# Performance work log

Hardware: AMD Instinct MI355X
Metric: run time of the kernel (lower is better)

## Reference

```python
import jax, jax.numpy as jnp
import numpy as np


def setup_inputs() -> dict:
    key = jax.random.key(0)
    k1, k2 = jax.random.split(key)
    N = 2_000_000
    rotation = jax.random.normal(k1, (N, 3, 3), dtype=jnp.float32)
    # learned parameter: eye(3) + 0.001 * randn(3,3)
    mat = jnp.eye(3, dtype=jnp.float32) + 0.001 * jax.random.normal(k2, (3, 3), dtype=jnp.float32)
    return {"rotation": rotation, "mat": mat}


def reference(rotation, mat):
    # new_mat[n] = rotation[n] @ mat   (mat broadcast over the batch)
    new_mat = jnp.einsum('nab,bc->nac', rotation, mat)
    # batched 3x3 SVD; polar orthogonal factor U @ V^T
    U, S, Vh = jnp.linalg.svd(new_mat, full_matrices=False)
    out = jnp.einsum('nab,nbc->nac', U, Vh)  # Vh is already V^T
    logdet = jnp.zeros((rotation.shape[0],), dtype=rotation.dtype)
    return out, logdet
```

## Files before the change

kernel.cpp:

```cpp
#include <hip/hip_runtime.h>
#include <math.h>

constexpr int BLOCK = 256;

__global__ __launch_bounds__(BLOCK) void polar3x3_kernel(
    const float* __restrict__ rot,
    const float* __restrict__ mat,
    float* __restrict__ outq,
    float* __restrict__ logdet,
    int N)
{
    const long long idx = (long long)blockIdx.x * BLOCK + threadIdx.x;
    if (idx >= N) return;

    const float* rp = rot + idx * 9;
    const float r0=rp[0], r1=rp[1], r2=rp[2], r3=rp[3], r4=rp[4],
                r5=rp[5], r6=rp[6], r7=rp[7], r8=rp[8];

    const float m0=mat[0], m1=mat[1], m2=mat[2], m3=mat[3], m4=mat[4],
                m5=mat[5], m6=mat[6], m7=mat[7], m8=mat[8];

    float x0 = fmaf(r0,m0, fmaf(r1,m3, r2*m6));
    float x1 = fmaf(r0,m1, fmaf(r1,m4, r2*m7));
    float x2 = fmaf(r0,m2, fmaf(r1,m5, r2*m8));
    float x3 = fmaf(r3,m0, fmaf(r4,m3, r5*m6));
    float x4 = fmaf(r3,m1, fmaf(r4,m4, r5*m7));
    float x5 = fmaf(r3,m2, fmaf(r4,m5, r5*m8));
    float x6 = fmaf(r6,m0, fmaf(r7,m3, r8*m6));
    float x7 = fmaf(r6,m1, fmaf(r7,m4, r8*m7));
    float x8 = fmaf(r6,m2, fmaf(r7,m5, r8*m8));

    const double dR = (double)r0*((double)r4*r8 - (double)r5*r7)
                    - (double)r1*((double)r3*r8 - (double)r5*r6)
                    + (double)r2*((double)r3*r7 - (double)r4*r6);
    const double dM = (double)m0*((double)m4*m8 - (double)m5*m7)
                    - (double)m1*((double)m3*m8 - (double)m5*m6)
                    + (double)m2*((double)m3*m7 - (double)m4*m6);
    const float detA = (float)(dR * dM);

    #pragma unroll
    for (int it = 0; it < 6; ++it) {
        const float c0 = fmaf(x4,x8, -x5*x7);
        const float c1 = fmaf(x5,x6, -x3*x8);
        const float c2 = fmaf(x3,x7, -x4*x6);
        const float c3 = fmaf(x2,x7, -x1*x8);
        const float c4 = fmaf(x0,x8, -x2*x6);
        const float c5 = fmaf(x1,x6, -x0*x7);
        const float c6 = fmaf(x1,x5, -x2*x4);
        const float c7 = fmaf(x2,x3, -x0*x5);
        const float c8 = fmaf(x0,x4, -x1*x3);
        const float det = (it == 0) ? detA
                        : fmaf(x0,c0, fmaf(x1,c1, x2*c2));
        const float adet = fmaxf(fabsf(det), 1e-30f);
        const float sdet = copysignf(adet, det);
        float nX2 = x0*x0;
        nX2 = fmaf(x1,x1, nX2); nX2 = fmaf(x2,x2, nX2);
        nX2 = fmaf(x3,x3, nX2); nX2 = fmaf(x4,x4, nX2);
        nX2 = fmaf(x5,x5, nX2); nX2 = fmaf(x6,x6, nX2);
        nX2 = fmaf(x7,x7, nX2); nX2 = fmaf(x8,x8, nX2);
        float nC2 = c0*c0;
        nC2 = fmaf(c1,c1, nC2); nC2 = fmaf(c2,c2, nC2);
        nC2 = fmaf(c3,c3, nC2); nC2 = fmaf(c4,c4, nC2);
        nC2 = fmaf(c5,c5, nC2); nC2 = fmaf(c6,c6, nC2);
        nC2 = fmaf(c7,c7, nC2); nC2 = fmaf(c8,c8, nC2);
        const float rr = nC2 * __builtin_amdgcn_rcpf(nX2);
        const float g  = __builtin_amdgcn_sqrtf(__builtin_amdgcn_sqrtf(rr))
                       * __builtin_amdgcn_rsqf(adet);
        const float s = 0.5f * g;
        const float t = 0.5f * __builtin_amdgcn_rcpf(g * sdet);
        x0 = fmaf(s,x0, t*c0); x1 = fmaf(s,x1, t*c1); x2 = fmaf(s,x2, t*c2);
        x3 = fmaf(s,x3, t*c3); x4 = fmaf(s,x4, t*c4); x5 = fmaf(s,x5, t*c5);
        x6 = fmaf(s,x6, t*c6); x7 = fmaf(s,x7, t*c7); x8 = fmaf(s,x8, t*c8);
    }

    float* op = outq + idx * 9;
    op[0]=x0; op[1]=x1; op[2]=x2; op[3]=x3; op[4]=x4;
    op[5]=x5; op[6]=x6; op[7]=x7; op[8]=x8;

    logdet[idx] = 0.0f;
}

extern "C" void kernel_launch(void* const* d_in, const int* in_sizes, int n_in,
                              void* d_out, int out_size, void* d_ws, size_t ws_size,
                              hipStream_t stream) {
    const float* rot = (const float*)d_in[0];
    const float* mat = (const float*)d_in[1];
    float* out = (float*)d_out;
    const int N = in_sizes[0] / 9;
    float* logdet = out + (long long)N * 9;
    const int nblocks = (N + BLOCK - 1) / BLOCK;
    polar3x3_kernel<<<nblocks, BLOCK, 0, stream>>>(rot, mat, out, logdet, N);
}
```

Baseline: 139.3 us.

## Process two matrices per thread with vector loads and nontemporal stores

Each thread now handles two consecutive 3x3 matrices. It loads and stores them as float2 vectors and uses nontemporal stores for the output and the logdet values. The Newton polar iteration is restructured into 5 scaled iterations followed by one unscaled final iteration. The scaling factors are computed with separate sqrt chains instead of a reciprocal of g*sdet. The intent is to widen memory transactions, add ILP by interleaving two independent matrices, and shorten the dependency chains. The cost is higher register pressure, and dropping the scaling on the last iteration could change accuracy.

```diff
diff --git a/kernel.cpp b/kernel.cpp
--- a/kernel.cpp
+++ b/kernel.cpp
@@ -1,5 +1,7 @@
 #include <hip/hip_runtime.h>
 #include <math.h>
+
+typedef float v2f __attribute__((ext_vector_type(2)));
 
 constexpr int BLOCK = 256;
 
@@ -10,74 +12,111 @@
     float* __restrict__ logdet,
     int N)
 {
-    const long long idx = (long long)blockIdx.x * BLOCK + threadIdx.x;
-    if (idx >= N) return;
+    const long long tid = (long long)blockIdx.x * BLOCK + threadIdx.x;
+    const long long i0 = tid * 2;
+    if (i0 >= N) return;
+    const bool full = (i0 + 1 < N);
 
-    const float* rp = rot + idx * 9;
-    const float r0=rp[0], r1=rp[1], r2=rp[2], r3=rp[3], r4=rp[4],
-                r5=rp[5], r6=rp[6], r7=rp[7], r8=rp[8];
+    float X[18];
+    if (full) {
+        const v2f* rp2 = (const v2f*)(rot + i0 * 9);
+        #pragma unroll
+        for (int k = 0; k < 9; ++k) { v2f w = rp2[k]; X[2*k] = w.x; X[2*k+1] = w.y; }
+    } else {
+        const float* rp = rot + i0 * 9;
+        #pragma unroll
+        for (int k = 0; k < 9; ++k) X[k] = rp[k];
+        #pragma unroll
+        for (int k = 9; k < 18; ++k) X[k] = 0.f;
+        X[9] = X[13] = X[17] = 1.f;
+    }
 
     const float m0=mat[0], m1=mat[1], m2=mat[2], m3=mat[3], m4=mat[4],
                 m5=mat[5], m6=mat[6], m7=mat[7], m8=mat[8];
+    const double dM = (double)m0*((double)m4*m8-(double)m5*m7)
+                    - (double)m1*((double)m3*m8-(double)m5*m6)
+                    + (double)m2*((double)m3*m7-(double)m4*m6);
 
-    float x0 = fmaf(r0,m0, fmaf(r1,m3, r2*m6));
-    float x1 = fmaf(r0,m1, fmaf(r1,m4, r2*m7));
-    float x2 = fmaf(r0,m2, fmaf(r1,m5, r2*m8));
-    float x3 = fmaf(r3,m0, fmaf(r4,m3, r5*m6));
-    float x4 = fmaf(r3,m1, fmaf(r4,m4, r5*m7));
-    float x5 = fmaf(r3,m2, fmaf(r4,m5, r5*m8));
-    float x6 = fmaf(r6,m0, fmaf(r7,m3, r8*m6));
-    float x7 = fmaf(r6,m1, fmaf(r7,m4, r8*m7));
-    float x8 = fmaf(r6,m2, fmaf(r7,m5, r8*m8));
-
-    const double dR = (double)r0*((double)r4*r8 - (double)r5*r7)
-                    - (double)r1*((double)r3*r8 - (double)r5*r6)
-                    + (double)r2*((double)r3*r7 - (double)r4*r6);
-    const double dM = (double)m0*((double)m4*m8 - (double)m5*m7)
-                    - (double)m1*((double)m3*m8 - (double)m5*m6)
-                    + (double)m2*((double)m3*m7 - (double)m4*m6);
-    const float detA = (float)(dR * dM);
+    float detA[2];
+    #pragma unroll
+    for (int j = 0; j < 2; ++j) {
+        float* p = &X[9*j];
+        const float r0=p[0],r1=p[1],r2=p[2],r3=p[3],r4=p[4],r5=p[5],r6=p[6],r7=p[7],r8=p[8];
+        const double dR = (double)r0*((double)r4*r8-(double)r5*r7)
+                        - (double)r1*((double)r3*r8-(double)r5*r6)
+                        + (double)r2*((double)r3*r7-(double)r4*r6);
+        detA[j] = (float)(dR * dM);
+        p[0]=fmaf(r0,m0,fmaf(r1,m3,r2*m6));
+        p[1]=fmaf(r0,m1,fmaf(r1,m4,r2*m7));
+        p[2]=fmaf(r0,m2,fmaf(r1,m5,r2*m8));
+        p[3]=fmaf(r3,m0,fmaf(r4,m3,r5*m6));
+        p[4]=fmaf(r3,m1,fmaf(r4,m4,r5*m7));
+        p[5]=fmaf(r3,m2,fmaf(r4,m5,r5*m8));
+        p[6]=fmaf(r6,m0,fmaf(r7,m3,r8*m6));
+        p[7]=fmaf(r6,m1,fmaf(r7,m4,r8*m7));
+        p[8]=fmaf(r6,m2,fmaf(r7,m5,r8*m8));
+    }
 
     #pragma unroll
-    for (int it = 0; it < 6; ++it) {
-        const float c0 = fmaf(x4,x8, -x5*x7);
-        const float c1 = fmaf(x5,x6, -x3*x8);
-        const float c2 = fmaf(x3,x7, -x4*x6);
-        const float c3 = fmaf(x2,x7, -x1*x8);
-        const float c4 = fmaf(x0,x8, -x2*x6);
-        const float c5 = fmaf(x1,x6, -x0*x7);
-        const float c6 = fmaf(x1,x5, -x2*x4);
-        const float c7 = fmaf(x2,x3, -x0*x5);
-        const float c8 = fmaf(x0,x4, -x1*x3);
-        const float det = (it == 0) ? detA
-                        : fmaf(x0,c0, fmaf(x1,c1, x2*c2));
-        const float adet = fmaxf(fabsf(det), 1e-30f);
-        const float sdet = copysignf(adet, det);
-        float nX2 = x0*x0;
-        nX2 = fmaf(x1,x1, nX2); nX2 = fmaf(x2,x2, nX2);
-        nX2 = fmaf(x3,x3, nX2); nX2 = fmaf(x4,x4, nX2);
-        nX2 = fmaf(x5,x5, nX2); nX2 = fmaf(x6,x6, nX2);
-        nX2 = fmaf(x7,x7, nX2); nX2 = fmaf(x8,x8, nX2);
-        float nC2 = c0*c0;
-        nC2 = fmaf(c1,c1, nC2); nC2 = fmaf(c2,c2, nC2);
-        nC2 = fmaf(c3,c3, nC2); nC2 = fmaf(c4,c4, nC2);
-        nC2 = fmaf(c5,c5, nC2); nC2 = fmaf(c6,c6, nC2);
-        nC2 = fmaf(c7,c7, nC2); nC2 = fmaf(c8,c8, nC2);
-        const float rr = nC2 * __builtin_amdgcn_rcpf(nX2);
-        const float g  = __builtin_amdgcn_sqrtf(__builtin_amdgcn_sqrtf(rr))
-                       * __builtin_amdgcn_rsqf(adet);
-        const float s = 0.5f * g;
-        const float t = 0.5f * __builtin_amdgcn_rcpf(g * sdet);
-        x0 = fmaf(s,x0, t*c0); x1 = fmaf(s,x1, t*c1); x2 = fmaf(s,x2, t*c2);
-        x3 = fmaf(s,x3, t*c3); x4 = fmaf(s,x4, t*c4); x5 = fmaf(s,x5, t*c5);
-        x6 = fmaf(s,x6, t*c6); x7 = fmaf(s,x7, t*c7); x8 = fmaf(s,x8, t*c8);
+    for (int it = 0; it < 5; ++it) {
+        #pragma unroll
+        for (int j = 0; j < 2; ++j) {
+            float* p = &X[9*j];
+            const float x0=p[0],x1=p[1],x2=p[2],x3=p[3],x4=p[4],x5=p[5],x6=p[6],x7=p[7],x8=p[8];
+            const float c0=fmaf(x4,x8,-x5*x7), c1=fmaf(x5,x6,-x3*x8), c2=fmaf(x3,x7,-x4*x6);
+            const float c3=fmaf(x2,x7,-x1*x8), c4=fmaf(x0,x8,-x2*x6), c5=fmaf(x1,x6,-x0*x7);
+            const float c6=fmaf(x1,x5,-x2*x4), c7=fmaf(x2,x3,-x0*x5), c8=fmaf(x0,x4,-x1*x3);
+            const float det = (it==0) ? detA[j] : fmaf(x0,c0,fmaf(x1,c1,x2*c2));
+            const float adet = fmaxf(fabsf(det), 1e-30f);
+            float nX2, nC2;
+            { const float a=fmaf(x1,x1,x0*x0), b=fmaf(x3,x3,x2*x2),
+                          e=fmaf(x5,x5,x4*x4), d=fmaf(x7,x7,x6*x6);
+              nX2=(a+b)+(e+fmaf(x8,x8,d)); }
+            { const float a=fmaf(c1,c1,c0*c0), b=fmaf(c3,c3,c2*c2),
+                          e=fmaf(c5,c5,c4*c4), d=fmaf(c7,c7,c6*c6);
+              nC2=(a+b)+(e+fmaf(c8,c8,d)); }
+            const float h  = __builtin_amdgcn_rsqf(adet);
+            const float pr = __builtin_amdgcn_sqrtf(__builtin_amdgcn_sqrtf(
+                                 nC2*__builtin_amdgcn_rcpf(nX2)));
+            const float qr = __builtin_amdgcn_sqrtf(__builtin_amdgcn_sqrtf(
+                                 nX2*__builtin_amdgcn_rcpf(nC2)));
+            const float s = 0.5f*pr*h;
+            const float t = copysignf(0.5f*qr*h, det);
+            p[0]=fmaf(s,x0,t*c0); p[1]=fmaf(s,x1,t*c1); p[2]=fmaf(s,x2,t*c2);
+            p[3]=fmaf(s,x3,t*c3); p[4]=fmaf(s,x4,t*c4); p[5]=fmaf(s,x5,t*c5);
+            p[6]=fmaf(s,x6,t*c6); p[7]=fmaf(s,x7,t*c7); p[8]=fmaf(s,x8,t*c8);
+        }
     }
 
-    float* op = outq + idx * 9;
-    op[0]=x0; op[1]=x1; op[2]=x2; op[3]=x3; op[4]=x4;
-    op[5]=x5; op[6]=x6; op[7]=x7; op[8]=x8;
+    #pragma unroll
+    for (int j = 0; j < 2; ++j) {
+        float* p = &X[9*j];
+        const float x0=p[0],x1=p[1],x2=p[2],x3=p[3],x4=p[4],x5=p[5],x6=p[6],x7=p[7],x8=p[8];
+        const float c0=fmaf(x4,x8,-x5*x7), c1=fmaf(x5,x6,-x3*x8), c2=fmaf(x3,x7,-x4*x6);
+        const float c3=fmaf(x2,x7,-x1*x8), c4=fmaf(x0,x8,-x2*x6), c5=fmaf(x1,x6,-x0*x7);
+        const float c6=fmaf(x1,x5,-x2*x4), c7=fmaf(x2,x3,-x0*x5), c8=fmaf(x0,x4,-x1*x3);
+        const float det = fmaf(x0,c0,fmaf(x1,c1,x2*c2));
+        const float t = 0.5f*__builtin_amdgcn_rcpf(det);
+        p[0]=fmaf(0.5f,x0,t*c0); p[1]=fmaf(0.5f,x1,t*c1); p[2]=fmaf(0.5f,x2,t*c2);
+        p[3]=fmaf(0.5f,x3,t*c3); p[4]=fmaf(0.5f,x4,t*c4); p[5]=fmaf(0.5f,x5,t*c5);
+        p[6]=fmaf(0.5f,x6,t*c6); p[7]=fmaf(0.5f,x7,t*c7); p[8]=fmaf(0.5f,x8,t*c8);
+    }
 
-    logdet[idx] = 0.0f;
+    float* op = outq + i0 * 9;
+    if (full) {
+        v2f* op2 = (v2f*)op;
+        #pragma unroll
+        for (int k = 0; k < 9; ++k) {
+            v2f w; w.x = X[2*k]; w.y = X[2*k+1];
+            __builtin_nontemporal_store(w, op2 + k);
+        }
+        v2f z; z.x = 0.f; z.y = 0.f;
+        __builtin_nontemporal_store(z, (v2f*)(logdet + i0));
+    } else {
+        #pragma unroll
+        for (int k = 0; k < 9; ++k) op[k] = X[k];
+        logdet[i0] = 0.f;
+    }
 }
 
 extern "C" void kernel_launch(void* const* d_in, const int* in_sizes, int n_in,
@@ -88,6 +127,7 @@
     float* out = (float*)d_out;
     const int N = in_sizes[0] / 9;
     float* logdet = out + (long long)N * 9;
-    const int nblocks = (N + BLOCK - 1) / BLOCK;
+    const long long nthreads = (N + 1) / 2;
+    const int nblocks = (int)((nthreads + BLOCK - 1) / BLOCK);
     polar3x3_kernel<<<nblocks, BLOCK, 0, stream>>>(rot, mat, out, logdet, N);
 }
```

After: 196.0 us. 1.41x slower.
